# Performance work log

Hardware: AMD Instinct MI355X
Metric: run time of the kernel (lower is better)

## Reference

```python
import jax, jax.numpy as jnp
import numpy as np

B, T, C = 2, 2048, 2048
N_HEAD, KV_HEADS = 16, 4
HEAD_DIM = C // N_HEAD  # 128
EPS = 1e-6


def setup_inputs() -> dict:
    key = jax.random.key(0)
    ks = jax.random.split(key, 3)
    x = jax.random.normal(ks[0], (B, T, C), dtype=jnp.float32)
    qkv_out = (N_HEAD + 2 * KV_HEADS) * HEAD_DIM  # 3072
    w_qkv = jax.random.normal(ks[1], (qkv_out, C), dtype=jnp.float32) * 0.02
    w_proj = jax.random.normal(ks[2], (C, C), dtype=jnp.float32) * 0.02
    q_norm_w = jnp.ones((HEAD_DIM,), dtype=jnp.float32)
    k_norm_w = jnp.ones((HEAD_DIM,), dtype=jnp.float32)
    # RoPE frequencies: theta = 10000^{-2i/d}, angles = pos * theta
    inv_freq = 1.0 / (10000.0 ** (np.arange(0, HEAD_DIM, 2, dtype=np.float32) / HEAD_DIM))
    angles = np.arange(T, dtype=np.float32)[:, None] * inv_freq[None, :]  # [T, 64]
    freqs_cos = jnp.asarray(np.cos(angles), dtype=jnp.float32)
    freqs_sin = jnp.asarray(np.sin(angles), dtype=jnp.float32)
    return {"x": x, "w_qkv": w_qkv, "w_proj": w_proj,
            "q_norm_w": q_norm_w, "k_norm_w": k_norm_w,
            "freqs_cos": freqs_cos, "freqs_sin": freqs_sin}


def _rope(t, cos, sin):
    # t: [B, H, T, D]; interpret last dim as D/2 complex pairs (a, b)
    a = t[..., 0::2]
    b = t[..., 1::2]
    oa = a * cos - b * sin
    ob = a * sin + b * cos
    return jnp.stack([oa, ob], axis=-1).reshape(t.shape)


def _rmsnorm(t, w, eps=EPS):
    rms = jnp.sqrt(jnp.mean(t * t, axis=-1, keepdims=True) + eps)
    return w * (t / rms)


def reference(x, w_qkv, w_proj, q_norm_w, k_norm_w, freqs_cos, freqs_sin):
    b, t, c = x.shape
    hd = HEAD_DIM
    qkv = x @ w_qkv.T  # [B, T, 3072]
    q_size = N_HEAD * hd
    kv_size = KV_HEADS * hd
    q = qkv[..., :q_size].reshape(b, t, N_HEAD, hd).transpose(0, 2, 1, 3)
    k = qkv[..., q_size:q_size + kv_size].reshape(b, t, KV_HEADS, hd).transpose(0, 2, 1, 3)
    v = qkv[..., q_size + kv_size:].reshape(b, t, KV_HEADS, hd).transpose(0, 2, 1, 3)
    # repeat_interleave KV heads to match query heads (GQA)
    rep = N_HEAD // KV_HEADS
    k = jnp.repeat(k, rep, axis=1)
    v = jnp.repeat(v, rep, axis=1)
    # RoPE (applied after repeat, matching the torch code order)
    cos = freqs_cos[:t][None, None, :, :]
    sin = freqs_sin[:t][None, None, :, :]
    q = _rope(q, cos, sin)
    k = _rope(k, cos, sin)
    # QK RMSNorm per head_dim
    q = _rmsnorm(q, q_norm_w)
    k = _rmsnorm(k, k_norm_w)
    # causal SDPA
    scores = jnp.einsum('bhqd,bhkd->bhqk', q, k) / jnp.sqrt(jnp.float32(hd))
    causal = jnp.tril(jnp.ones((t, t), dtype=bool))
    scores = jnp.where(causal[None, None], scores, jnp.finfo(scores.dtype).min)
    att = jax.nn.softmax(scores, axis=-1)
    y = jnp.einsum('bhqk,bhkd->bhqd', att, v)
    y = y.transpose(0, 2, 1, 3).reshape(b, t, c)
    return y @ w_proj.T
```

## Files before the change

kernel.cpp:

```cpp
#include <hip/hip_runtime.h>
#include <hip/hip_bf16.h>

#define B_    2
#define T_    2048
#define C_    2048
#define NH_   16
#define KVH_  4
#define HD_   128
#define QKV_  3072
#define M_    4096

typedef float  floatx4 __attribute__((ext_vector_type(4)));
typedef __bf16 bf16x8  __attribute__((ext_vector_type(8)));
typedef __bf16 bf16x4  __attribute__((ext_vector_type(4)));
typedef __bf16 bf16x2  __attribute__((ext_vector_type(2)));

typedef const __attribute__((address_space(1))) void* gas_t;
typedef __attribute__((address_space(3))) void*       las_t;
__device__ __forceinline__ void gl_lds16(const void* g, void* l) {
  __builtin_amdgcn_global_load_lds((gas_t)g, (las_t)l, 16, 0, 0);
}

__global__ __launch_bounds__(256) void cvt3(const float* __restrict__ s0, __bf16* __restrict__ d0, int n0,
                                            const float* __restrict__ s1, __bf16* __restrict__ d1, int n1,
                                            const float* __restrict__ s2, __bf16* __restrict__ d2, int n2) {
  int i = blockIdx.x * blockDim.x + threadIdx.x;
  const float* s; __bf16* d;
  if (i < n0) { s = s0; d = d0; }
  else {
    i -= n0;
    if (i < n1) { s = s1; d = d1; }
    else { i -= n1; if (i >= n2) return; s = s2; d = d2; }
  }
  float4 f = ((const float4*)s)[i];
  bf16x4 o = { (__bf16)f.x, (__bf16)f.y, (__bf16)f.z, (__bf16)f.w };
  ((bf16x4*)d)[i] = o;
}

template <typename OutT>
__global__ __launch_bounds__(256, 2) void gemm_cnt(const __bf16* __restrict__ A,
                                                   const __bf16* __restrict__ Bm,
                                                   OutT* __restrict__ Cc,
                                                   int N, int K) {
  __shared__ __align__(16) __bf16 As[2][128 * 64];
  __shared__ __align__(16) __bf16 Bs[2][128 * 64];
  const int tid  = threadIdx.x;
  const int wid  = tid >> 6, lane = tid & 63, quad = lane >> 4, r16 = lane & 15;
  const int bm   = blockIdx.y * 128, bn = blockIdx.x * 128;
  const int wm   = (wid >> 1) * 64, wn = (wid & 1) * 64;
  const int srow = tid >> 3;
  const int clog = (tid & 7) ^ (srow & 7);
  const __bf16* aR = A  + (size_t)(bm + srow) * K + clog * 8;
  const __bf16* bR = Bm + (size_t)(bn + srow) * K + clog * 8;
  const int nt = K >> 6;

  floatx4 acc[4][4];
  #pragma unroll
  for (int i = 0; i < 4; i++)
    #pragma unroll
    for (int j = 0; j < 4; j++) acc[i][j] = (floatx4){0.f, 0.f, 0.f, 0.f};

  auto stage = [&](int s, int k0) {
    #pragma unroll
    for (int p = 0; p < 4; p++) {
      gl_lds16(aR + (size_t)(p * 32) * K + k0, &As[s][(p * 32 + wid * 8) * 64]);
      gl_lds16(bR + (size_t)(p * 32) * K + k0, &Bs[s][(p * 32 + wid * 8) * 64]);
    }
  };

  stage(0, 0);

  #pragma unroll 1
  for (int j = 0; j < nt; ++j) {
    if (j + 1 < nt) {
      stage((j + 1) & 1, (j + 1) << 6);
      asm volatile("s_waitcnt vmcnt(8)" ::: "memory");
    } else {
      asm volatile("s_waitcnt vmcnt(0)" ::: "memory");
    }
    __builtin_amdgcn_s_barrier();
    asm volatile("" ::: "memory");

    const __bf16* Ab = As[j & 1];
    const __bf16* Bb = Bs[j & 1];
    #pragma unroll
    for (int hf = 0; hf < 2; hf++) {
      const int xo = (((hf << 2) + quad) ^ (r16 & 7)) << 3;
      bf16x8 af[4], bfr[4];
      #pragma unroll
      for (int i = 0; i < 4; i++) af[i]  = *(const bf16x8*)&Ab[(wm + i * 16 + r16) * 64 + xo];
      #pragma unroll
      for (int i = 0; i < 4; i++) bfr[i] = *(const bf16x8*)&Bb[(wn + i * 16 + r16) * 64 + xo];
      __builtin_amdgcn_s_setprio(1);
      #pragma unroll
      for (int i = 0; i < 4; i++)
        #pragma unroll
        for (int jj = 0; jj < 4; jj++)
          acc[i][jj] = __builtin_amdgcn_mfma_f32_16x16x32_bf16(af[i], bfr[jj], acc[i][jj], 0, 0, 0);
      __builtin_amdgcn_s_setprio(0);
    }
    asm volatile("" ::: "memory");
    __builtin_amdgcn_s_barrier();
    asm volatile("" ::: "memory");
  }

  #pragma unroll
  for (int i = 0; i < 4; i++) {
    #pragma unroll
    for (int reg = 0; reg < 4; reg++) {
      int row = bm + wm + i * 16 + quad * 4 + reg;
      OutT* crow = Cc + (size_t)row * N + bn + wn;
      #pragma unroll
      for (int j = 0; j < 4; j++) crow[j * 16 + r16] = (OutT)acc[i][j][reg];
    }
  }
}

__global__ __launch_bounds__(256) void ropevt(const __bf16* __restrict__ qkv,
                                              const float* __restrict__ qw,
                                              const float* __restrict__ kw,
                                              const float* __restrict__ fc,
                                              const float* __restrict__ fs,
                                              __bf16* __restrict__ qn,
                                              __bf16* __restrict__ kn,
                                              __bf16* __restrict__ vT) {
  __shared__ __bf16 L[64 * 68];
  const int tid = threadIdx.x;
  if (blockIdx.x < M_ / 4) {
    const int wid  = tid >> 6, lane = tid & 63;
    const int row  = blockIdx.x * 4 + wid;
    const int b    = row >> 11, t = row & (T_ - 1);
    const float cs = fc[t * 64 + lane], sn = fs[t * 64 + lane];
    const __bf16* base = qkv + (size_t)row * QKV_;

    #pragma unroll 2
    for (int h = 0; h < NH_; h++) {
      bf16x2 ab = *(const bf16x2*)(base + h * HD_ + 2 * lane);
      float ax = (float)ab[0], ay = (float)ab[1];
      float oa = ax * cs - ay * sn;
      float ob = ax * sn + ay * cs;
      float ss = oa * oa + ob * ob;
      #pragma unroll
      for (int off = 32; off; off >>= 1) ss += __shfl_xor(ss, off);
      float rinv = rsqrtf(ss * (1.0f / HD_) + 1e-6f);
      bf16x2 o = { (__bf16)(oa * rinv * qw[2 * lane]), (__bf16)(ob * rinv * qw[2 * lane + 1]) };
      *(bf16x2*)&qn[(size_t)((b * NH_ + h) * T_ + t) * HD_ + 2 * lane] = o;
    }
    #pragma unroll 2
    for (int h = 0; h < KVH_; h++) {
      bf16x2 ab = *(const bf16x2*)(base + C_ + h * HD_ + 2 * lane);
      float ax = (float)ab[0], ay = (float)ab[1];
      float oa = ax * cs - ay * sn;
      float ob = ax * sn + ay * cs;
      float ss = oa * oa + ob * ob;
      #pragma unroll
      for (int off = 32; off; off >>= 1) ss += __shfl_xor(ss, off);
      float rinv = rsqrtf(ss * (1.0f / HD_) + 1e-6f);
      bf16x2 o = { (__bf16)(oa * rinv * kw[2 * lane]), (__bf16)(ob * rinv * kw[2 * lane + 1]) };
      *(bf16x2*)&kn[(size_t)((b * KVH_ + h) * T_ + t) * HD_ + 2 * lane] = o;
    }
    return;
  }
  const int idx = blockIdx.x - M_ / 4;
  const int t0 = (idx & 31) * 64;
  const int d0 = ((idx >> 5) & 1) * 64;
  const int z  = idx >> 6;
  const int b  = z >> 2, hk = z & 3;
  const int srcc = C_ + KVH_ * HD_ + hk * HD_ + d0;
  const int rr = tid >> 4, c4 = (tid & 15) * 4;
  #pragma unroll
  for (int i = 0; i < 4; i++) {
    int t = rr + i * 16;
    bf16x4 f = *(const bf16x4*)&qkv[(size_t)(b * T_ + t0 + t) * QKV_ + srcc + c4];
    *(bf16x4*)&L[t * 68 + c4] = f;
  }
  __syncthreads();
  const int dr = tid >> 3, tc8 = (tid & 7) * 8;
  #pragma unroll
  for (int i = 0; i < 2; i++) {
    int d = dr + i * 32;
    bf16x8 ov;
    #pragma unroll
    for (int j = 0; j < 8; j++) ov[j] = L[(tc8 + j) * 68 + d];
    *(bf16x8*)&vT[(size_t)(z * HD_ + d0 + d) * T_ + t0 + tc8] = ov;
  }
}

__device__ __forceinline__ int swz_w(int lane) {
  return ((lane & 3) << 4) | ((lane >> 2) ^ ((lane & 3) << 1));
}
__device__ __forceinline__ int swz_r(int quad, int r16) {
  return (quad << 4) | (r16 ^ (quad << 1));
}

__device__ __forceinline__ void kv_prefetch8(const __bf16* kbase, const __bf16* vbase,
                                             int kt0, int wid, int lane,
                                             bf16x8 kreg[2], bf16x8 vreg[2]) {
  const int r4 = lane >> 2, c8 = (lane & 3) * 8;
  #pragma unroll
  for (int i = 0; i < 2; i++) {
    const int n = wid * 2 + i;
    kreg[i] = *(const bf16x8*)&kbase[(size_t)(kt0 + (n >> 2) * 16 + r4) * HD_ + (n & 3) * 32 + c8];
    vreg[i] = *(const bf16x8*)&vbase[(size_t)((n >> 1) * 16 + r4) * T_ + kt0 + (n & 1) * 32 + c8];
  }
}

__device__ __forceinline__ void kv_commit8(__bf16* Ks, __bf16* Vs, int wid, int lane,
                                           const bf16x8 kreg[2], const bf16x8 vreg[2]) {
  const int slot = swz_w(lane);
  #pragma unroll
  for (int i = 0; i < 2; i++) {
    *(bf16x8*)(Ks + (wid * 2 + i) * 512 + slot * 8) = kreg[i];
    *(bf16x8*)(Vs + (wid * 2 + i) * 512 + slot * 8) = vreg[i];
  }
}

__global__ __launch_bounds__(512, 4) void flash(const __bf16* __restrict__ q,
                                                const __bf16* __restrict__ k,
                                                const __bf16* __restrict__ vT,
                                                __bf16* __restrict__ y) {
  __shared__ __align__(16) __bf16 Ks[2][64 * 128];
  __shared__ __align__(16) __bf16 Vs[2][64 * 128];
  __shared__ __align__(16) __bf16 Ps[8][16 * 48];
  const int tid = threadIdx.x;
  const int wid = tid >> 6, lane = tid & 63, quad = lane >> 4, r16 = lane & 15;
  const int x   = blockIdx.x;
  const int p   = (x >> 5) & 7, hl = x & 31;
  const int qt  = (x < 256) ? (15 - p) : p;
  const int b = hl >> 4, h = hl & 15, hk = h >> 2;

  const __bf16* kbase = k  + (size_t)(b * KVH_ + hk) * T_ * HD_;
  const __bf16* vbase = vT + (size_t)(b * KVH_ + hk) * HD_ * T_;
  __bf16* Pw = Ps[wid];
  const float sc = 0.08838834764831845f;
  const float NEG = -__builtin_inff();
  bf16x8 ones;
  #pragma unroll
  for (int i = 0; i < 8; i++) ones[i] = (__bf16)1.0f;

  const int nt = 2 * (qt + 1);
  const int r0 = qt * 128 + wid * 16;

  const __bf16* qrow = q + ((size_t)(b * NH_ + h) * T_ + r0 + r16) * HD_;
  bf16x8 qf[4];
  #pragma unroll
  for (int kb = 0; kb < 4; kb++) qf[kb] = *(const bf16x8*)&qrow[kb * 32 + quad * 8];

  floatx4 o[8], ol = (floatx4){0.f, 0.f, 0.f, 0.f};
  #pragma unroll
  for (int j = 0; j < 8; j++) o[j] = (floatx4){0.f, 0.f, 0.f, 0.f};
  float m_r[4] = {NEG, NEG, NEG, NEG};

  bf16x8 kreg[2], vreg[2];
  kv_prefetch8(kbase, vbase, 0, wid, lane, kreg, vreg);
  kv_commit8(&Ks[0][0], &Vs[0][0], wid, lane, kreg, vreg);
  if (nt > 1) kv_prefetch8(kbase, vbase, 64, wid, lane, kreg, vreg);
  __syncthreads();

  #pragma unroll 1
  for (int it = 0; it < nt; ++it) {
    if (it + 1 < nt) {
      kv_commit8(&Ks[(it + 1) & 1][0], &Vs[(it + 1) & 1][0], wid, lane, kreg, vreg);
      if (it + 2 < nt) kv_prefetch8(kbase, vbase, (it + 2) * 64, wid, lane, kreg, vreg);
    }

    const int kt0 = it * 64;
    const __bf16* Kb = &Ks[it & 1][0];
    const __bf16* Vb = &Vs[it & 1][0];
    if (kt0 <= r0 + 15) {
      floatx4 s[4];
      #pragma unroll
      for (int cb = 0; cb < 4; cb++) s[cb] = (floatx4){0.f, 0.f, 0.f, 0.f};
      __builtin_amdgcn_s_setprio(1);
      #pragma unroll
      for (int kb = 0; kb < 4; kb++)
        #pragma unroll
        for (int cb = 0; cb < 4; cb++) {
          bf16x8 kf = *(const bf16x8*)&Kb[(cb * 4 + kb) * 512 + swz_r(quad, r16) * 8];
          s[cb] = __builtin_amdgcn_mfma_f32_16x16x32_bf16(qf[kb], kf, s[cb], 0, 0, 0);
        }
      __builtin_amdgcn_s_setprio(0);

      const bool needmask = (kt0 + 63 > r0);
      #pragma unroll
      for (int reg = 0; reg < 4; reg++) {
        const int rowq = r0 + quad * 4 + reg;
        s[0][reg] *= sc; s[1][reg] *= sc; s[2][reg] *= sc; s[3][reg] *= sc;
        if (needmask) {
          if (kt0 +      r16 > rowq) s[0][reg] = NEG;
          if (kt0 + 16 + r16 > rowq) s[1][reg] = NEG;
          if (kt0 + 32 + r16 > rowq) s[2][reg] = NEG;
          if (kt0 + 48 + r16 > rowq) s[3][reg] = NEG;
        }
      }
      float mx[4], mnew[4];
      #pragma unroll
      for (int reg = 0; reg < 4; reg++) {
        float m0 = fmaxf(fmaxf(s[0][reg], s[1][reg]), fmaxf(s[2][reg], s[3][reg]));
        #pragma unroll
        for (int off = 8; off; off >>= 1) m0 = fmaxf(m0, __shfl_xor(m0, off));
        mx[reg] = m0;
        mnew[reg] = fmaxf(m_r[reg], m0);
      }
      float growth = fmaxf(fmaxf(mx[0] - m_r[0], mx[1] - m_r[1]),
                           fmaxf(mx[2] - m_r[2], mx[3] - m_r[3]));
      if (!__all(growth <= 8.0f)) {
        #pragma unroll
        for (int reg = 0; reg < 4; reg++) {
          float a = __expf(m_r[reg] - mnew[reg]);
          m_r[reg] = mnew[reg];
          ol[reg] *= a;
          #pragma unroll
          for (int j = 0; j < 8; j++) o[j][reg] *= a;
        }
      }
      #pragma unroll
      for (int c = 0; c < 2; c++) {
        #pragma unroll
        for (int reg = 0; reg < 4; reg++) {
          const int prow = quad * 4 + reg;
          Pw[prow * 48 +      r16] = (__bf16)__expf(s[2 * c    ][reg] - m_r[reg]);
          Pw[prow * 48 + 16 + r16] = (__bf16)__expf(s[2 * c + 1][reg] - m_r[reg]);
        }
        __asm__ volatile("" ::: "memory");
        bf16x8 pf = *(const bf16x8*)&Pw[r16 * 48 + quad * 8];
        __builtin_amdgcn_s_setprio(1);
        ol = __builtin_amdgcn_mfma_f32_16x16x32_bf16(pf, ones, ol, 0, 0, 0);
        #pragma unroll
        for (int j = 0; j < 8; j++) {
          bf16x8 vf = *(const bf16x8*)&Vb[(j * 2 + c) * 512 + swz_r(quad, r16) * 8];
          o[j] = __builtin_amdgcn_mfma_f32_16x16x32_bf16(pf, vf, o[j], 0, 0, 0);
        }
        __builtin_amdgcn_s_setprio(0);
        __asm__ volatile("" ::: "memory");
      }
    }
    __syncthreads();
  }

  #pragma unroll
  for (int reg = 0; reg < 4; reg++) {
    int trow = r0 + quad * 4 + reg;
    float inv = 1.0f / ol[reg];
    __bf16* yr = y + ((size_t)(b * T_) + trow) * C_ + h * HD_;
    #pragma unroll
    for (int j = 0; j < 8; j++) yr[j * 16 + r16] = (__bf16)(o[j][reg] * inv);
  }
}

extern "C" void kernel_launch(void* const* d_in, const int* in_sizes, int n_in,
                              void* d_out, int out_size, void* d_ws, size_t ws_size,
                              hipStream_t stream) {
  const float* x     = (const float*)d_in[0];
  const float* wqkv  = (const float*)d_in[1];
  const float* wproj = (const float*)d_in[2];
  const float* qw    = (const float*)d_in[3];
  const float* kw    = (const float*)d_in[4];
  const float* fc    = (const float*)d_in[5];
  const float* fs    = (const float*)d_in[6];
  float* out = (float*)d_out;

  char* w = (char*)d_ws;
  __bf16* xb     = (__bf16*)w; w += (size_t)M_ * C_ * 2;
  __bf16* wqkvb  = (__bf16*)w; w += (size_t)QKV_ * C_ * 2;
  __bf16* wprojb = (__bf16*)w; w += (size_t)C_ * C_ * 2;
  __bf16* qkv    = (__bf16*)w; w += (size_t)M_ * QKV_ * 2;
  __bf16* qn     = (__bf16*)w; w += (size_t)B_ * NH_ * T_ * HD_ * 2;
  __bf16* kn     = (__bf16*)w; w += (size_t)B_ * KVH_ * T_ * HD_ * 2;
  __bf16* vT     = (__bf16*)w; w += (size_t)B_ * KVH_ * T_ * HD_ * 2;
  __bf16* ybf    = (__bf16*)w; w += (size_t)M_ * C_ * 2;

  const int n0 = M_ * C_ / 4, n1 = QKV_ * C_ / 4, n2 = C_ * C_ / 4;
  cvt3<<<(n0 + n1 + n2 + 255) / 256, 256, 0, stream>>>(x, xb, n0, wqkv, wqkvb, n1, wproj, wprojb, n2);

  gemm_cnt<__bf16><<<dim3(QKV_ / 128, M_ / 128), 256, 0, stream>>>(xb, wqkvb, qkv, QKV_, C_);
  ropevt<<<M_ / 4 + (T_ / 64) * (HD_ / 64) * (B_ * KVH_), 256, 0, stream>>>(qkv, qw, kw, fc, fs, qn, kn, vT);
  flash<<<dim3(512), 512, 0, stream>>>(qn, kn, vT, ybf);
  gemm_cnt<float><<<dim3(C_ / 128, M_ / 128), 256, 0, stream>>>(ybf, wprojb, out, C_, C_);
}
```

Before: 316.0 us.

## Shrink flash query tile to 64 rows with single-buffered KV and 1024 blocks

The flash kernel moves from 128-row query tiles with 8 waves and double-buffered K/V LDS to 64-row tiles with 4 waves, single-buffered K/V held in registers across iterations, and twice as many blocks. Block scheduling now pairs long and short causal tiles across four bands to balance work. The aim is to cut LDS use, wasted causal tiles and load imbalance, and to raise the number of resident blocks. The cost is an extra __syncthreads per iteration and each block reusing a loaded K/V tile for fewer query rows.

New measurement: 307.2 us. -2.8%, faster.

```diff
diff --git a/kernel.cpp b/kernel.cpp
--- a/kernel.cpp
+++ b/kernel.cpp
@@ -193,41 +193,43 @@
   return (quad << 4) | (r16 ^ (quad << 1));
 }
 
-__device__ __forceinline__ void kv_prefetch8(const __bf16* kbase, const __bf16* vbase,
-                                             int kt0, int wid, int lane,
-                                             bf16x8 kreg[2], bf16x8 vreg[2]) {
+__device__ __forceinline__ void kv_prefetch16(const __bf16* kbase, const __bf16* vbase,
+                                              int kt0, int wid, int lane,
+                                              bf16x8 kreg[4], bf16x8 vreg[4]) {
   const int r4 = lane >> 2, c8 = (lane & 3) * 8;
   #pragma unroll
-  for (int i = 0; i < 2; i++) {
-    const int n = wid * 2 + i;
+  for (int i = 0; i < 4; i++) {
+    const int n = wid * 4 + i;
     kreg[i] = *(const bf16x8*)&kbase[(size_t)(kt0 + (n >> 2) * 16 + r4) * HD_ + (n & 3) * 32 + c8];
     vreg[i] = *(const bf16x8*)&vbase[(size_t)((n >> 1) * 16 + r4) * T_ + kt0 + (n & 1) * 32 + c8];
   }
 }
 
-__device__ __forceinline__ void kv_commit8(__bf16* Ks, __bf16* Vs, int wid, int lane,
-                                           const bf16x8 kreg[2], const bf16x8 vreg[2]) {
+__device__ __forceinline__ void kv_commit16(__bf16* Ks, __bf16* Vs, int wid, int lane,
+                                            const bf16x8 kreg[4], const bf16x8 vreg[4]) {
   const int slot = swz_w(lane);
   #pragma unroll
-  for (int i = 0; i < 2; i++) {
-    *(bf16x8*)(Ks + (wid * 2 + i) * 512 + slot * 8) = kreg[i];
-    *(bf16x8*)(Vs + (wid * 2 + i) * 512 + slot * 8) = vreg[i];
-  }
-}
-
-__global__ __launch_bounds__(512, 4) void flash(const __bf16* __restrict__ q,
+  for (int i = 0; i < 4; i++) {
+    *(bf16x8*)(Ks + (wid * 4 + i) * 512 + slot * 8) = kreg[i];
+    *(bf16x8*)(Vs + (wid * 4 + i) * 512 + slot * 8) = vreg[i];
+  }
+}
+
+__global__ __launch_bounds__(256, 3) void flash(const __bf16* __restrict__ q,
                                                 const __bf16* __restrict__ k,
                                                 const __bf16* __restrict__ vT,
                                                 __bf16* __restrict__ y) {
-  __shared__ __align__(16) __bf16 Ks[2][64 * 128];
-  __shared__ __align__(16) __bf16 Vs[2][64 * 128];
-  __shared__ __align__(16) __bf16 Ps[8][16 * 48];
+  __shared__ __align__(16) __bf16 Ks[64 * 128];
+  __shared__ __align__(16) __bf16 Vs[128 * 64];
+  __shared__ __align__(16) __bf16 Ps[4][16 * 48];
   const int tid = threadIdx.x;
   const int wid = tid >> 6, lane = tid & 63, quad = lane >> 4, r16 = lane & 15;
   const int x   = blockIdx.x;
-  const int p   = (x >> 5) & 7, hl = x & 31;
-  const int qt  = (x < 256) ? (15 - p) : p;
-  const int b = hl >> 4, h = hl & 15, hk = h >> 2;
+  const int g   = x >> 5, bh = x & 31;
+  const int sub = g & 7, band = g >> 3;
+  const int qp  = (band == 0) ? (31 - sub) : (band == 1) ? (16 + sub)
+                : (band == 2) ? (15 - sub) : sub;
+  const int b = bh >> 4, h = bh & 15, hk = h >> 2;
 
   const __bf16* kbase = k  + (size_t)(b * KVH_ + hk) * T_ * HD_;
   const __bf16* vbase = vT + (size_t)(b * KVH_ + hk) * HD_ * T_;
@@ -238,8 +240,8 @@
   #pragma unroll
   for (int i = 0; i < 8; i++) ones[i] = (__bf16)1.0f;
 
-  const int nt = 2 * (qt + 1);
-  const int r0 = qt * 128 + wid * 16;
+  const int nt = qp + 1;
+  const int r0 = qp * 64 + wid * 16;
 
   const __bf16* qrow = q + ((size_t)(b * NH_ + h) * T_ + r0 + r16) * HD_;
   bf16x8 qf[4];
@@ -251,23 +253,18 @@
   for (int j = 0; j < 8; j++) o[j] = (floatx4){0.f, 0.f, 0.f, 0.f};
   float m_r[4] = {NEG, NEG, NEG, NEG};
 
-  bf16x8 kreg[2], vreg[2];
-  kv_prefetch8(kbase, vbase, 0, wid, lane, kreg, vreg);
-  kv_commit8(&Ks[0][0], &Vs[0][0], wid, lane, kreg, vreg);
-  if (nt > 1) kv_prefetch8(kbase, vbase, 64, wid, lane, kreg, vreg);
-  __syncthreads();
+  bf16x8 kreg[4], vreg[4];
+  kv_prefetch16(kbase, vbase, 0, wid, lane, kreg, vreg);
 
   #pragma unroll 1
   for (int it = 0; it < nt; ++it) {
-    if (it + 1 < nt) {
-      kv_commit8(&Ks[(it + 1) & 1][0], &Vs[(it + 1) & 1][0], wid, lane, kreg, vreg);
-      if (it + 2 < nt) kv_prefetch8(kbase, vbase, (it + 2) * 64, wid, lane, kreg, vreg);
-    }
+    __syncthreads();
+    kv_commit16(Ks, Vs, wid, lane, kreg, vreg);
+    __syncthreads();
+    if (it + 1 < nt) kv_prefetch16(kbase, vbase, (it + 1) * 64, wid, lane, kreg, vreg);
 
     const int kt0 = it * 64;
-    const __bf16* Kb = &Ks[it & 1][0];
-    const __bf16* Vb = &Vs[it & 1][0];
-    if (kt0 <= r0 + 15) {
+    {
       floatx4 s[4];
       #pragma unroll
       for (int cb = 0; cb < 4; cb++) s[cb] = (floatx4){0.f, 0.f, 0.f, 0.f};
@@ -276,7 +273,7 @@
       for (int kb = 0; kb < 4; kb++)
         #pragma unroll
         for (int cb = 0; cb < 4; cb++) {
-          bf16x8 kf = *(const bf16x8*)&Kb[(cb * 4 + kb) * 512 + swz_r(quad, r16) * 8];
+          bf16x8 kf = *(const bf16x8*)&Ks[(cb * 4 + kb) * 512 + swz_r(quad, r16) * 8];
           s[cb] = __builtin_amdgcn_mfma_f32_16x16x32_bf16(qf[kb], kf, s[cb], 0, 0, 0);
         }
       __builtin_amdgcn_s_setprio(0);
@@ -328,14 +325,13 @@
         ol = __builtin_amdgcn_mfma_f32_16x16x32_bf16(pf, ones, ol, 0, 0, 0);
         #pragma unroll
         for (int j = 0; j < 8; j++) {
-          bf16x8 vf = *(const bf16x8*)&Vb[(j * 2 + c) * 512 + swz_r(quad, r16) * 8];
+          bf16x8 vf = *(const bf16x8*)&Vs[(j * 2 + c) * 512 + swz_r(quad, r16) * 8];
           o[j] = __builtin_amdgcn_mfma_f32_16x16x32_bf16(pf, vf, o[j], 0, 0, 0);
         }
         __builtin_amdgcn_s_setprio(0);
         __asm__ volatile("" ::: "memory");
       }
     }
-    __syncthreads();
   }
 
   #pragma unroll
@@ -375,6 +371,6 @@
 
   gemm_cnt<__bf16><<<dim3(QKV_ / 128, M_ / 128), 256, 0, stream>>>(xb, wqkvb, qkv, QKV_, C_);
   ropevt<<<M_ / 4 + (T_ / 64) * (HD_ / 64) * (B_ * KVH_), 256, 0, stream>>>(qkv, qw, kw, fc, fs, qn, kn, vT);
-  flash<<<dim3(512), 512, 0, stream>>>(qn, kn, vT, ybf);
+  flash<<<dim3(1024), 256, 0, stream>>>(qn, kn, vT, ybf);
   gemm_cnt<float><<<dim3(C_ / 128, M_ / 128), 256, 0, stream>>>(ybf, wprojb, out, C_, C_);
 }
```
